# Optimization experiments

Measured on AMD Instinct MI355X. Metric: run time of the kernel, lower is better.

Reference implementation:

```python
import jax, jax.numpy as jnp
import numpy as np

N_NODES = 100000
N_EDGES = 1600000
IN_C = 128
DIM = 64
OUT_C = 64
BN_EPS = 1e-5


def _batchnorm(x, g, b):
    # training-mode BatchNorm1d: batch mean, biased variance
    m = jnp.mean(x, axis=0)
    v = jnp.var(x, axis=0)
    return (x - m) * jax.lax.rsqrt(v + BN_EPS) * g + b


def setup_inputs() -> dict:
    key = jax.random.key(0)
    ks = jax.random.split(key, 16)
    s = lambda fan: 1.0 / np.sqrt(fan)
    inp = {
        "X": jax.random.normal(ks[0], (N_NODES, IN_C), dtype=jnp.float32),
        "edge_index": jax.random.randint(ks[1], (2, N_EDGES), 0, N_NODES, dtype=jnp.int32),
        "edge_attr": jax.random.normal(ks[2], (N_EDGES, 1), dtype=jnp.float32),
        # bn_in over in_channels
        "bn_in_g": jnp.ones((IN_C,), jnp.float32),
        "bn_in_b": jnp.zeros((IN_C,), jnp.float32),
        # layer 0: edge lin 1->IN_C, node MLP IN_C->DIM
        "We0": jax.random.normal(ks[3], (1, IN_C), jnp.float32) * s(1),
        "be0": jnp.zeros((IN_C,), jnp.float32),
        "W0": jax.random.normal(ks[4], (IN_C, DIM), jnp.float32) * s(IN_C),
        "b0": jnp.zeros((DIM,), jnp.float32),
        "bn0_g": jnp.ones((DIM,), jnp.float32),
        "bn0_b": jnp.zeros((DIM,), jnp.float32),
        # layer 1: edge lin 1->DIM, node MLP DIM->DIM
        "We1": jax.random.normal(ks[5], (1, DIM), jnp.float32) * s(1),
        "be1": jnp.zeros((DIM,), jnp.float32),
        "W1": jax.random.normal(ks[6], (DIM, DIM), jnp.float32) * s(DIM),
        "b1": jnp.zeros((DIM,), jnp.float32),
        "bn1_g": jnp.ones((DIM,), jnp.float32),
        "bn1_b": jnp.zeros((DIM,), jnp.float32),
        # fc1: DIM->OUT_C, no bias
        "Wfc": jax.random.normal(ks[7], (DIM, OUT_C), jnp.float32) * s(DIM),
    }
    return inp


def reference(X, edge_index, edge_attr,
              bn_in_g, bn_in_b,
              We0, be0, W0, b0, bn0_g, bn0_b,
              We1, be1, W1, b1, bn1_g, bn1_b,
              Wfc):
    n = X.shape[0]
    src, dst = edge_index[0], edge_index[1]

    def gine(x, We, be, W, b):
        # GINEConv with eps=0: tanh(Linear(x + sum_j relu(x_j + lin(e_ij))))
        e = edge_attr @ We + be            # [E, C]
        msg = jax.nn.relu(x[src] + e)      # gather + edge-add + relu
        agg = jax.ops.segment_sum(msg, dst, num_segments=n)  # scatter-sum
        return jnp.tanh((x + agg) @ W + b)

    x = _batchnorm(X, bn_in_g, bn_in_b)
    h1 = _batchnorm(gine(x, We0, be0, W0, b0), bn0_g, bn0_b)
    h2 = _batchnorm(gine(h1, We1, be1, W1, b1), bn1_g, bn1_b)
    h3 = jnp.tanh(h2 @ Wfc)
    return jnp.concatenate([h1, h2, h3], axis=-1)  # [N, DIM+DIM+OUT_C]
```

## Files before the change

### kernel.cpp

```cpp
#include <hip/hip_runtime.h>
#include <hip/hip_fp16.h>
#include <math.h>
#include <stdint.h>

#define NN 100000
#define NE 1600000
#define INC 128
#define DIM 64
#define EPS 1e-5f
#define SB 512
#define NREP 8
#define NPART 8
#define PART_SZ ((NN + NPART - 1) / NPART)

struct __align__(8)  half4 { __half2 a, b; };
struct __align__(16) half8 { __half2 a, b, c, d; };

__global__ __launch_bounds__(256) void stats_hist_kernel(const float* __restrict__ X,
        const int* __restrict__ dst, int* __restrict__ counts,
        double* __restrict__ sum_out, double* __restrict__ sq_out) {
    __shared__ double ls[256], lq[256];
    if (blockIdx.x < SB) {
        int c  = threadIdx.x & 127;
        int rl = threadIdx.x >> 7;
        int row = blockIdx.x * 2 + rl;
        const int rstride = SB * 2;
        double s = 0.0, q = 0.0;
        for (int r = row; r < NN; r += rstride) {
            double v = (double)X[(size_t)r * INC + c];
            s += v; q += v * v;
        }
        ls[threadIdx.x] = s; lq[threadIdx.x] = q;
        __syncthreads();
        if (rl == 0) {
            s += ls[128 + c]; q += lq[128 + c];
            int rep = blockIdx.x & (NREP - 1);
            atomicAdd(&sum_out[rep * INC + c], s);
            atomicAdd(&sq_out[rep * INC + c], q);
        }
    } else {
        int e = (blockIdx.x - SB) * 256 + threadIdx.x;
        if (e < NE) atomicAdd(&counts[dst[e]], 1);
    }
}

template<int C>
__device__ inline void bn_fold_rep(int t, const double* dsum, const double* dsq,
                                   const float* g, const float* b, float* sc_s, float* sh_s) {
    if (t < C) {
        double s = 0.0, q = 0.0;
        #pragma unroll
        for (int r = 0; r < NREP; r++) { s += dsum[r * C + t]; q += dsq[r * C + t]; }
        double m = s / (double)NN;
        double v = q / (double)NN - m * m;
        double sc = (double)g[t] / sqrt(v + (double)EPS);
        sc_s[t] = (float)sc;
        sh_s[t] = (float)((double)b[t] - m * sc);
    }
}

__global__ __launch_bounds__(256) void xhat_half_kernel(const float* __restrict__ X,
        const double* __restrict__ dsum, const double* __restrict__ dsq,
        const float* __restrict__ g, const float* __restrict__ b,
        __half* __restrict__ Xh) {
    __shared__ float sc_s[INC], sh_s[INC];
    bn_fold_rep<INC>(threadIdx.x, dsum, dsq, g, b, sc_s, sh_s);
    __syncthreads();
    size_t i = (size_t)blockIdx.x * 256 + threadIdx.x;
    size_t e4 = i * 4;
    if (e4 >= (size_t)NN * INC) return;
    int c = (int)(e4 & 127);
    float4 x = *(const float4*)(X + e4);
    half4 h;
    h.a = __floats2half2_rn(fmaf(x.x, sc_s[c], sh_s[c]), fmaf(x.y, sc_s[c + 1], sh_s[c + 1]));
    h.b = __floats2half2_rn(fmaf(x.z, sc_s[c + 2], sh_s[c + 2]), fmaf(x.w, sc_s[c + 3], sh_s[c + 3]));
    *(half4*)(Xh + e4) = h;
}

__global__ __launch_bounds__(1024) void scan1_kernel(const int* __restrict__ counts,
                                                     int* __restrict__ offs, int* __restrict__ bsums) {
    __shared__ int tmp[2][1024];
    int t = threadIdx.x;
    int g = blockIdx.x * 1024 + t;
    int v = (g < NN) ? counts[g] : 0;
    tmp[0][t] = v;
    __syncthreads();
    int pin = 0;
    for (int d = 1; d < 1024; d <<= 1) {
        int x = tmp[pin][t] + ((t >= d) ? tmp[pin][t - d] : 0);
        tmp[pin ^ 1][t] = x;
        pin ^= 1;
        __syncthreads();
    }
    int incl = tmp[pin][t];
    if (g < NN) offs[g] = incl - v;
    if (t == 1023) bsums[blockIdx.x] = incl;
}

__global__ __launch_bounds__(128) void scan2_kernel(int* __restrict__ bsums, int nb) {
    __shared__ int tmp[2][128];
    int t = threadIdx.x;
    int v = (t < nb) ? bsums[t] : 0;
    tmp[0][t] = v;
    __syncthreads();
    int pin = 0;
    for (int d = 1; d < 128; d <<= 1) {
        int x = tmp[pin][t] + ((t >= d) ? tmp[pin][t - d] : 0);
        tmp[pin ^ 1][t] = x;
        pin ^= 1;
        __syncthreads();
    }
    if (t < nb) bsums[t] = tmp[pin][t] - v;
}

__global__ __launch_bounds__(256) void scan3_kernel(int* __restrict__ offs, const int* __restrict__ bsums,
                                                    int* __restrict__ cursor) {
    int g = blockIdx.x * 256 + threadIdx.x;
    if (g < NN) {
        int o = offs[g] + bsums[g >> 10];
        offs[g] = o;
        cursor[g] = o;
    }
    if (g == 0) offs[NN] = NE;
}

__global__ __launch_bounds__(256) void scatter_kernel(const int* __restrict__ src, const int* __restrict__ dst,
                                                      const float* __restrict__ ea, int* __restrict__ cursor,
                                                      int2* __restrict__ src_ea) {
    const int p = blockIdx.x & (NPART - 1);
    const int blk = blockIdx.x >> 3;
    const int nblk = gridDim.x >> 3;
    const int lo = p * PART_SZ;
    const int hi = min(NN, lo + PART_SZ);
    for (int e = blk * 256 + threadIdx.x; e < NE; e += nblk * 256) {
        int d = dst[e];
        if (d >= lo && d < hi) {
            int pos = atomicAdd(&cursor[d], 1);
            src_ea[pos] = make_int2(src[e], __float_as_int(ea[e]));
        }
    }
}

__global__ __launch_bounds__(512, 8) void gine0_kernel(const float* __restrict__ X,
        const __half* __restrict__ Xh,
        const int* __restrict__ offs, const int2* __restrict__ src_ea,
        const double* __restrict__ dsum, const double* __restrict__ dsq,
        const float* __restrict__ g, const float* __restrict__ b,
        const float* __restrict__ We, const float* __restrict__ be,
        const float* __restrict__ W, const float* __restrict__ bvec,
        __half* __restrict__ t1h, double* __restrict__ dsum0, double* __restrict__ dsq0) {
    __shared__ __align__(16) float  u_s[32][INC + 4];
    __shared__ __align__(16) __half w_sh[DIM][INC + 8];
    __shared__ float sc_s[INC], sh_s[INC];
    const int t = threadIdx.x;
    const int row0 = blockIdx.x * 32;
    bn_fold_rep<INC>(t, dsum, dsq, g, b, sc_s, sh_s);
    for (int i = t; i < INC * DIM; i += 512) {
        int k = i >> 6, c = i & 63;
        w_sh[c][k] = __float2half_rn(W[i]);
    }
    __syncthreads();
    const int wid = t >> 6, l = t & 63;
    const int quarter = l >> 4;
    const int c8 = (l & 15) * 8;
    float4 wv0 = *(const float4*)(We + c8);
    float4 wv1 = *(const float4*)(We + c8 + 4);
    float4 bv0 = *(const float4*)(be + c8);
    float4 bv1 = *(const float4*)(be + c8 + 4);

    #define G0_ACC(vh, av)  do { \
        float2 f0 = __half22float2((vh).a), f1 = __half22float2((vh).b); \
        float2 f2 = __half22float2((vh).c), f3 = __half22float2((vh).d); \
        a0 += fmaxf(f0.x + fmaf((av), wv0.x, bv0.x), 0.f); \
        a1 += fmaxf(f0.y + fmaf((av), wv0.y, bv0.y), 0.f); \
        a2 += fmaxf(f1.x + fmaf((av), wv0.z, bv0.z), 0.f); \
        a3 += fmaxf(f1.y + fmaf((av), wv0.w, bv0.w), 0.f); \
        a4 += fmaxf(f2.x + fmaf((av), wv1.x, bv1.x), 0.f); \
        a5 += fmaxf(f2.y + fmaf((av), wv1.y, bv1.y), 0.f); \
        a6 += fmaxf(f3.x + fmaf((av), wv1.z, bv1.z), 0.f); \
        a7 += fmaxf(f3.y + fmaf((av), wv1.w, bv1.w), 0.f); \
    } while (0)

    for (int nn = 0; nn < 4; ++nn) {
        int r = wid * 4 + nn;
        int n = row0 + r;
        float a0 = 0.f, a1 = 0.f, a2 = 0.f, a3 = 0.f, a4 = 0.f, a5 = 0.f, a6 = 0.f, a7 = 0.f;
        if (n < NN) {
            int beg = offs[n], end = offs[n + 1];
            for (int base = beg; base < end; base += 64) {
                int j = base + l;
                int2 p = (j < end) ? src_ea[j] : make_int2(0, 0);
                float avf = __int_as_float(p.y);
                int cnt = min(64, end - base);
                int tt = 0;
                for (; tt + 8 <= cnt; tt += 8) {
                    int e0 = tt + quarter, e1 = tt + 4 + quarter;
                    int s0 = __shfl(p.x, e0), s1 = __shfl(p.x, e1);
                    float av0 = __shfl(avf, e0), av1 = __shfl(avf, e1);
                    half8 v0 = *(const half8*)(Xh + (size_t)s0 * INC + c8);
                    half8 v1 = *(const half8*)(Xh + (size_t)s1 * INC + c8);
                    G0_ACC(v0, av0); G0_ACC(v1, av1);
                }
                for (; tt < cnt; tt += 4) {
                    int e0 = tt + quarter;
                    int es = min(e0, cnt - 1);
                    int s0 = __shfl(p.x, es);
                    float av0 = __shfl(avf, es);
                    if (e0 < cnt) {
                        half8 v0 = *(const half8*)(Xh + (size_t)s0 * INC + c8);
                        G0_ACC(v0, av0);
                    }
                }
            }
        }
        a0 += __shfl_xor(a0, 16); a0 += __shfl_xor(a0, 32);
        a1 += __shfl_xor(a1, 16); a1 += __shfl_xor(a1, 32);
        a2 += __shfl_xor(a2, 16); a2 += __shfl_xor(a2, 32);
        a3 += __shfl_xor(a3, 16); a3 += __shfl_xor(a3, 32);
        a4 += __shfl_xor(a4, 16); a4 += __shfl_xor(a4, 32);
        a5 += __shfl_xor(a5, 16); a5 += __shfl_xor(a5, 32);
        a6 += __shfl_xor(a6, 16); a6 += __shfl_xor(a6, 32);
        a7 += __shfl_xor(a7, 16); a7 += __shfl_xor(a7, 32);
        if (quarter == 0) {
            if (n < NN) {
                float4 x0 = *(const float4*)(X + (size_t)n * INC + c8);
                float4 x1 = *(const float4*)(X + (size_t)n * INC + c8 + 4);
                a0 += fmaf(x0.x, sc_s[c8],     sh_s[c8]);
                a1 += fmaf(x0.y, sc_s[c8 + 1], sh_s[c8 + 1]);
                a2 += fmaf(x0.z, sc_s[c8 + 2], sh_s[c8 + 2]);
                a3 += fmaf(x0.w, sc_s[c8 + 3], sh_s[c8 + 3]);
                a4 += fmaf(x1.x, sc_s[c8 + 4], sh_s[c8 + 4]);
                a5 += fmaf(x1.y, sc_s[c8 + 5], sh_s[c8 + 5]);
                a6 += fmaf(x1.z, sc_s[c8 + 6], sh_s[c8 + 6]);
                a7 += fmaf(x1.w, sc_s[c8 + 7], sh_s[c8 + 7]);
            }
            *(float4*)&u_s[r][c8]     = make_float4(a0, a1, a2, a3);
            *(float4*)&u_s[r][c8 + 4] = make_float4(a4, a5, a6, a7);
        }
    }
    #undef G0_ACC
    __syncthreads();
    const int cc = t & 15;
    const int rg = t >> 4;
    float acc0 = bvec[cc], acc1 = bvec[cc + 16], acc2 = bvec[cc + 32], acc3 = bvec[cc + 48];
    #pragma unroll 2
    for (int k = 0; k < INC; k += 8) {
        float4 ua = *(const float4*)&u_s[rg][k];
        float4 ub = *(const float4*)&u_s[rg][k + 4];
        half8 w0 = *(const half8*)&w_sh[cc][k];
        half8 w1 = *(const half8*)&w_sh[cc + 16][k];
        half8 w2 = *(const half8*)&w_sh[cc + 32][k];
        half8 w3 = *(const half8*)&w_sh[cc + 48][k];
        float2 p;
        p = __half22float2(w0.a); acc0 = fmaf(ua.x, p.x, fmaf(ua.y, p.y, acc0));
        p = __half22float2(w0.b); acc0 = fmaf(ua.z, p.x, fmaf(ua.w, p.y, acc0));
        p = __half22float2(w0.c); acc0 = fmaf(ub.x, p.x, fmaf(ub.y, p.y, acc0));
        p = __half22float2(w0.d); acc0 = fmaf(ub.z, p.x, fmaf(ub.w, p.y, acc0));
        p = __half22float2(w1.a); acc1 = fmaf(ua.x, p.x, fmaf(ua.y, p.y, acc1));
        p = __half22float2(w1.b); acc1 = fmaf(ua.z, p.x, fmaf(ua.w, p.y, acc1));
        p = __half22float2(w1.c); acc1 = fmaf(ub.x, p.x, fmaf(ub.y, p.y, acc1));
        p = __half22float2(w1.d); acc1 = fmaf(ub.z, p.x, fmaf(ub.w, p.y, acc1));
        p = __half22float2(w2.a); acc2 = fmaf(ua.x, p.x, fmaf(ua.y, p.y, acc2));
        p = __half22float2(w2.b); acc2 = fmaf(ua.z, p.x, fmaf(ua.w, p.y, acc2));
        p = __half22float2(w2.c); acc2 = fmaf(ub.x, p.x, fmaf(ub.y, p.y, acc2));
        p = __half22float2(w2.d); acc2 = fmaf(ub.z, p.x, fmaf(ub.w, p.y, acc2));
        p = __half22float2(w3.a); acc3 = fmaf(ua.x, p.x, fmaf(ua.y, p.y, acc3));
        p = __half22float2(w3.b); acc3 = fmaf(ua.z, p.x, fmaf(ua.w, p.y, acc3));
        p = __half22float2(w3.c); acc3 = fmaf(ub.x, p.x, fmaf(ub.y, p.y, acc3));
        p = __half22float2(w3.d); acc3 = fmaf(ub.z, p.x, fmaf(ub.w, p.y, acc3));
    }
    int rr = row0 + rg;
    float t0 = tanhf(acc0), t1v = tanhf(acc1), t2v = tanhf(acc2), t3v = tanhf(acc3);
    if (rr < NN) {
        __half* op = t1h + (size_t)rr * DIM;
        op[cc]      = __float2half_rn(t0);
        op[cc + 16] = __float2half_rn(t1v);
        op[cc + 32] = __float2half_rn(t2v);
        op[cc + 48] = __float2half_rn(t3v);
    }
    __syncthreads();
    float* red_s = (float*)u_s;
    float* red_q = red_s + 2048;
    bool ok = (rr < NN);
    red_s[rg * 64 + cc]      = ok ? t0 : 0.f;
    red_s[rg * 64 + cc + 16] = ok ? t1v : 0.f;
    red_s[rg * 64 + cc + 32] = ok ? t2v : 0.f;
    red_s[rg * 64 + cc + 48] = ok ? t3v : 0.f;
    red_q[rg * 64 + cc]      = ok ? t0 * t0 : 0.f;
    red_q[rg * 64 + cc + 16] = ok ? t1v * t1v : 0.f;
    red_q[rg * 64 + cc + 32] = ok ? t2v * t2v : 0.f;
    red_q[rg * 64 + cc + 48] = ok ? t3v * t3v : 0.f;
    __syncthreads();
    if (t < 64) {
        float s = 0.f, q = 0.f;
        #pragma unroll
        for (int i = 0; i < 32; i++) { s += red_s[i * 64 + t]; q += red_q[i * 64 + t]; }
        int rep = blockIdx.x & (NREP - 1);
        atomicAdd(&dsum0[rep * DIM + t], (double)s);
        atomicAdd(&dsq0[rep * DIM + t], (double)q);
    }
}

__global__ __launch_bounds__(512) void gine1_kernel(const __half* __restrict__ t1h,
        const int* __restrict__ offs, const int2* __restrict__ src_ea,
        const double* __restrict__ dsum, const double* __restrict__ dsq,
        const float* __restrict__ g, const float* __restrict__ b,
        const float* __restrict__ We, const float* __restrict__ be,
        const float* __restrict__ W, const float* __restrict__ bvec,
        float* __restrict__ out, double* __restrict__ dsum1, double* __restrict__ dsq1) {
    __shared__ __align__(16) float u_s[64][DIM + 4];
    __shared__ __align__(16) float w_s[DIM][DIM + 4];
    __shared__ float sc_s[DIM], sh_s[DIM];
    const int t = threadIdx.x;
    const int row0 = blockIdx.x * 64;
    bn_fold_rep<DIM>(t, dsum, dsq, g, b, sc_s, sh_s);
    for (int i = t; i < DIM * DIM; i += 512) {
        int k = i >> 6, c = i & 63;
        w_s[c][k] = W[i];
    }
    __syncthreads();
    const int wid = t >> 6, l = t & 63;
    const int quarter = l >> 4;
    const int c4 = (l & 15) * 4;
    float4 wv = *(const float4*)(We + c4);
    float4 bv = *(const float4*)(be + c4);
    float4 sc4 = *(const float4*)(sc_s + c4);
    float4 sh4 = *(const float4*)(sh_s + c4);

    #define G1_ACC(vh, av)  do { \
        float2 f00 = __half22float2((vh).a), f01 = __half22float2((vh).b); \
        a0 += fmaxf(fmaf(f00.x, sc4.x, sh4.x) + fmaf((av), wv.x, bv.x), 0.f); \
        a1 += fmaxf(fmaf(f00.y, sc4.y, sh4.y) + fmaf((av), wv.y, bv.y), 0.f); \
        a2 += fmaxf(fmaf(f01.x, sc4.z, sh4.z) + fmaf((av), wv.z, bv.z), 0.f); \
        a3 += fmaxf(fmaf(f01.y, sc4.w, sh4.w) + fmaf((av), wv.w, bv.w), 0.f); \
    } while (0)

    for (int nn = 0; nn < 8; ++nn) {
        int r = wid * 8 + nn;
        int n = row0 + r;
        float a0 = 0.f, a1 = 0.f, a2 = 0.f, a3 = 0.f;
        if (n < NN) {
            int beg = offs[n], end = offs[n + 1];
            for (int base = beg; base < end; base += 64) {
                int j = base + l;
                int2 p = (j < end) ? src_ea[j] : make_int2(0, 0);
                float avf = __int_as_float(p.y);
                int cnt = min(64, end - base);
                int tt = 0;
                for (; tt + 8 <= cnt; tt += 8) {
                    int e0 = tt + quarter, e1 = tt + 4 + quarter;
                    int s0 = __shfl(p.x, e0), s1 = __shfl(p.x, e1);
                    float av0 = __shfl(avf, e0), av1 = __shfl(avf, e1);
                    half4 v0 = *(const half4*)(t1h + (size_t)s0 * DIM + c4);
                    half4 v1 = *(const half4*)(t1h + (size_t)s1 * DIM + c4);
                    G1_ACC(v0, av0); G1_ACC(v1, av1);
                }
                for (; tt < cnt; tt += 4) {
                    int e0 = tt + quarter;
                    int es = min(e0, cnt - 1);
                    int s0 = __shfl(p.x, es);
                    float av0 = __shfl(avf, es);
                    if (e0 < cnt) {
                        half4 v0 = *(const half4*)(t1h + (size_t)s0 * DIM + c4);
                        G1_ACC(v0, av0);
                    }
                }
            }
        }
        a0 += __shfl_xor(a0, 16); a0 += __shfl_xor(a0, 32);
        a1 += __shfl_xor(a1, 16); a1 += __shfl_xor(a1, 32);
        a2 += __shfl_xor(a2, 16); a2 += __shfl_xor(a2, 32);
        a3 += __shfl_xor(a3, 16); a3 += __shfl_xor(a3, 32);
        if (quarter == 0) {
            if (n < NN) {
                half4 h = *(const half4*)(t1h + (size_t)n * DIM + c4);
                float2 f0 = __half22float2(h.a), f1 = __half22float2(h.b);
                float h0 = fmaf(f0.x, sc4.x, sh4.x);
                float h1 = fmaf(f0.y, sc4.y, sh4.y);
                float h2 = fmaf(f1.x, sc4.z, sh4.z);
                float h3 = fmaf(f1.y, sc4.w, sh4.w);
                *(float4*)(out + (size_t)n * 192 + c4) = make_float4(h0, h1, h2, h3);
                a0 += h0; a1 += h1; a2 += h2; a3 += h3;
            }
            *(float4*)&u_s[r][c4] = make_float4(a0, a1, a2, a3);
        }
    }
    #undef G1_ACC
    __syncthreads();
    const int cc = t & 15;
    const int r0 = (t >> 4) * 2;
    float acc[2][4];
    #pragma unroll
    for (int j = 0; j < 4; j++) {
        float bj = bvec[cc + 16 * j];
        acc[0][j] = bj; acc[1][j] = bj;
    }
    #pragma unroll 4
    for (int k = 0; k < DIM; k += 4) {
        float4 w0 = *(const float4*)&w_s[cc][k];
        float4 w1 = *(const float4*)&w_s[cc + 16][k];
        float4 w2 = *(const float4*)&w_s[cc + 32][k];
        float4 w3 = *(const float4*)&w_s[cc + 48][k];
        #pragma unroll
        for (int i = 0; i < 2; i++) {
            float4 u = *(const float4*)&u_s[r0 + i][k];
            acc[i][0] = fmaf(u.x, w0.x, fmaf(u.y, w0.y, fmaf(u.z, w0.z, fmaf(u.w, w0.w, acc[i][0]))));
            acc[i][1] = fmaf(u.x, w1.x, fmaf(u.y, w1.y, fmaf(u.z, w1.z, fmaf(u.w, w1.w, acc[i][1]))));
            acc[i][2] = fmaf(u.x, w2.x, fmaf(u.y, w2.y, fmaf(u.z, w2.z, fmaf(u.w, w2.w, acc[i][2]))));
            acc[i][3] = fmaf(u.x, w3.x, fmaf(u.y, w3.y, fmaf(u.z, w3.z, fmaf(u.w, w3.w, acc[i][3]))));
        }
    }
    float tv[2][4];
    #pragma unroll
    for (int i = 0; i < 2; i++) {
        int rr = row0 + r0 + i;
        #pragma unroll
        for (int j = 0; j < 4; j++) tv[i][j] = tanhf(acc[i][j]);
        if (rr < NN) {
            float* op = out + (size_t)rr * 192 + 64;
            #pragma unroll
            for (int j = 0; j < 4; j++) op[cc + 16 * j] = tv[i][j];
        }
    }
    __syncthreads();
    float* red_s = (float*)w_s;
    float* red_q = red_s + 2048;
    const int rgp = t >> 4;
    bool ok0 = (row0 + r0 < NN), ok1 = (row0 + r0 + 1 < NN);
    #pragma unroll
    for (int j = 0; j < 4; j++) {
        float v0 = ok0 ? tv[0][j] : 0.f;
        float v1 = ok1 ? tv[1][j] : 0.f;
        red_s[rgp * 64 + cc + 16 * j] = v0 + v1;
        red_q[rgp * 64 + cc + 16 * j] = v0 * v0 + v1 * v1;
    }
    __syncthreads();
    if (t < 64) {
        float s = 0.f, q = 0.f;
        #pragma unroll
        for (int i = 0; i < 32; i++) { s += red_s[i * 64 + t]; q += red_q[i * 64 + t]; }
        int rep = blockIdx.x & (NREP - 1);
        atomicAdd(&dsum1[rep * DIM + t], (double)s);
        atomicAdd(&dsq1[rep * DIM + t], (double)q);
    }
}

__global__ __launch_bounds__(256) void fc_kernel(float* __restrict__ io,
        const double* __restrict__ dsum, const double* __restrict__ dsq,
        const float* __restrict__ g, const float* __restrict__ b,
        const float* __restrict__ W) {
    __shared__ __align__(16) float u_s[64][DIM + 4];
    __shared__ __align__(16) float w_s[DIM][DIM + 4];
    __shared__ float sc_s[DIM], sh_s[DIM];
    const int t = threadIdx.x;
    const int row0 = blockIdx.x * 64;
    bn_fold_rep<DIM>(t, dsum, dsq, g, b, sc_s, sh_s);
    __syncthreads();
    for (int i = t; i < DIM * DIM; i += 256) {
        int k = i >> 6, c = i & 63;
        w_s[c][k] = W[i];
    }
    for (int i = t; i < 64 * DIM; i += 256) {
        int r = i >> 6, k = i & 63;
        int rr = row0 + r;
        float v = 0.f;
        if (rr < NN) {
            size_t idx = (size_t)rr * 192 + 64 + k;
            v = fmaf(io[idx], sc_s[k], sh_s[k]);
            io[idx] = v;
        }
        u_s[r][k] = v;
    }
    __syncthreads();
    const int cc = t & 15;
    const int r0 = (t >> 4) << 2;
    float acc[4][4];
    #pragma unroll
    for (int j = 0; j < 4; j++) { acc[0][j] = 0.f; acc[1][j] = 0.f; acc[2][j] = 0.f; acc[3][j] = 0.f; }
    #pragma unroll 4
    for (int k = 0; k < DIM; k += 4) {
        float4 w0 = *(const float4*)&w_s[cc][k];
        float4 w1 = *(const float4*)&w_s[cc + 16][k];
        float4 w2 = *(const float4*)&w_s[cc + 32][k];
        float4 w3 = *(const float4*)&w_s[cc + 48][k];
        #pragma unroll
        for (int i = 0; i < 4; i++) {
            float4 u = *(const float4*)&u_s[r0 + i][k];
            acc[i][0] = fmaf(u.x, w0.x, fmaf(u.y, w0.y, fmaf(u.z, w0.z, fmaf(u.w, w0.w, acc[i][0]))));
            acc[i][1] = fmaf(u.x, w1.x, fmaf(u.y, w1.y, fmaf(u.z, w1.z, fmaf(u.w, w1.w, acc[i][1]))));
            acc[i][2] = fmaf(u.x, w2.x, fmaf(u.y, w2.y, fmaf(u.z, w2.z, fmaf(u.w, w2.w, acc[i][2]))));
            acc[i][3] = fmaf(u.x, w3.x, fmaf(u.y, w3.y, fmaf(u.z, w3.z, fmaf(u.w, w3.w, acc[i][3]))));
        }
    }
    #pragma unroll
    for (int i = 0; i < 4; i++) {
        int rr = row0 + r0 + i;
        if (rr < NN) {
            #pragma unroll
            for (int j = 0; j < 4; j++)
                io[(size_t)rr * 192 + 128 + cc + 16 * j] = tanhf(acc[i][j]);
        }
    }
}

extern "C" void kernel_launch(void* const* d_in, const int* in_sizes, int n_in,
                              void* d_out, int out_size, void* d_ws, size_t ws_size,
                              hipStream_t stream) {
    const float* X      = (const float*)d_in[0];
    const int*   ei     = (const int*)  d_in[1];
    const float* ea     = (const float*)d_in[2];
    const float* bng    = (const float*)d_in[3];
    const float* bnb    = (const float*)d_in[4];
    const float* We0    = (const float*)d_in[5];
    const float* be0    = (const float*)d_in[6];
    const float* W0     = (const float*)d_in[7];
    const float* b0     = (const float*)d_in[8];
    const float* bn0g   = (const float*)d_in[9];
    const float* bn0b   = (const float*)d_in[10];
    const float* We1    = (const float*)d_in[11];
    const float* be1    = (const float*)d_in[12];
    const float* W1     = (const float*)d_in[13];
    const float* b1     = (const float*)d_in[14];
    const float* bn1g   = (const float*)d_in[15];
    const float* bn1b   = (const float*)d_in[16];
    const float* Wfc    = (const float*)d_in[17];

    const int* src = ei;
    const int* dst = ei + NE;
    float* out = (float*)d_out;

    int2*   src_ea  = (int2*)d_ws;
    __half* t1h     = (__half*)(src_ea + NE);
    __half* Xh      = t1h + (size_t)NN * DIM;
    int*    counts  = (int*)(Xh + (size_t)NN * INC);
    int*    offs    = counts + NN;
    int*    cursor  = offs + NN + 1;
    int*    bsums   = cursor + NN;
    double* dstats = (double*)(((uintptr_t)(bsums + 128) + 15) & ~(uintptr_t)15);
    double* dsum_in = dstats;
    double* dsq_in  = dsum_in + NREP * INC;
    double* dsum0   = dsq_in + NREP * INC;
    double* dsq0    = dsum0 + NREP * DIM;
    double* dsum1   = dsq0 + NREP * DIM;
    double* dsq1    = dsum1 + NREP * DIM;
    const size_t nstats = (size_t)NREP * (2 * INC + 4 * DIM);

    hipMemsetAsync(counts, 0, NN * sizeof(int), stream);
    hipMemsetAsync(dstats, 0, nstats * sizeof(double), stream);

    stats_hist_kernel<<<SB + (NE + 255) / 256, 256, 0, stream>>>(X, dst, counts, dsum_in, dsq_in);

    xhat_half_kernel<<<(NN * INC / 4 + 255) / 256, 256, 0, stream>>>(X, dsum_in, dsq_in, bng, bnb, Xh);

    const int NB = (NN + 1023) / 1024;
    scan1_kernel<<<NB, 1024, 0, stream>>>(counts, offs, bsums);
    scan2_kernel<<<1, 128, 0, stream>>>(bsums, NB);
    scan3_kernel<<<(NN + 255) / 256, 256, 0, stream>>>(offs, bsums, cursor);
    scatter_kernel<<<2048, 256, 0, stream>>>(src, dst, ea, cursor, src_ea);

    gine0_kernel<<<(NN + 31) / 32, 512, 0, stream>>>(X, Xh, offs, src_ea, dsum_in, dsq_in, bng, bnb,
                                                     We0, be0, W0, b0, t1h, dsum0, dsq0);

    gine1_kernel<<<(NN + 63) / 64, 512, 0, stream>>>(t1h, offs, src_ea, dsum0, dsq0, bn0g, bn0b,
                                                     We1, be1, W1, b1, out, dsum1, dsq1);

    fc_kernel<<<(NN + 63) / 64, 256, 0, stream>>>(out, dsum1, dsq1, bn1g, bn1b, Wfc);
}
```

Baseline: 442.8 us.

## Replicate degree histogram and accumulate layer-0 messages in packed fp16

The degree histogram is split into NREP replicated copies chosen by block index, so atomics from different blocks hit different copies. The first scan sums the copies back together. The layer-0 gather loop now computes the edge embedding, ReLU and accumulation in packed half2 arithmetic (v_pk_max_f16, hfma2) instead of converting to fp32. This cuts ALU work per edge, but accumulating sums of about 16 or more messages in fp16 loses precision and risks tolerance failures. The larger counts buffer also needs a larger memset and more reads in the scan.

```diff
diff --git a/kernel.cpp b/kernel.cpp
--- a/kernel.cpp
+++ b/kernel.cpp
@@ -15,6 +15,12 @@
 
 struct __align__(8)  half4 { __half2 a, b; };
 struct __align__(16) half8 { __half2 a, b, c, d; };
+
+__device__ inline __half2 h2max(__half2 a, __half2 b) {
+    __half2 r;
+    asm("v_pk_max_f16 %0, %1, %2" : "=v"(r) : "v"(a), "v"(b));
+    return r;
+}
 
 __global__ __launch_bounds__(256) void stats_hist_kernel(const float* __restrict__ X,
         const int* __restrict__ dst, int* __restrict__ counts,
@@ -39,8 +45,9 @@
             atomicAdd(&sq_out[rep * INC + c], q);
         }
     } else {
-        int e = (blockIdx.x - SB) * 256 + threadIdx.x;
-        if (e < NE) atomicAdd(&counts[dst[e]], 1);
+        int bb = blockIdx.x - SB;
+        int e = bb * 256 + threadIdx.x;
+        if (e < NE) atomicAdd(&counts[(bb & (NREP - 1)) * NN + dst[e]], 1);
     }
 }
 
@@ -82,7 +89,11 @@
     __shared__ int tmp[2][1024];
     int t = threadIdx.x;
     int g = blockIdx.x * 1024 + t;
-    int v = (g < NN) ? counts[g] : 0;
+    int v = 0;
+    if (g < NN) {
+        #pragma unroll
+        for (int r = 0; r < NREP; r++) v += counts[r * NN + g];
+    }
     tmp[0][t] = v;
     __syncthreads();
     int pin = 0;
@@ -163,28 +174,27 @@
     const int wid = t >> 6, l = t & 63;
     const int quarter = l >> 4;
     const int c8 = (l & 15) * 8;
-    float4 wv0 = *(const float4*)(We + c8);
-    float4 wv1 = *(const float4*)(We + c8 + 4);
-    float4 bv0 = *(const float4*)(be + c8);
-    float4 bv1 = *(const float4*)(be + c8 + 4);
-
-    #define G0_ACC(vh, av)  do { \
-        float2 f0 = __half22float2((vh).a), f1 = __half22float2((vh).b); \
-        float2 f2 = __half22float2((vh).c), f3 = __half22float2((vh).d); \
-        a0 += fmaxf(f0.x + fmaf((av), wv0.x, bv0.x), 0.f); \
-        a1 += fmaxf(f0.y + fmaf((av), wv0.y, bv0.y), 0.f); \
-        a2 += fmaxf(f1.x + fmaf((av), wv0.z, bv0.z), 0.f); \
-        a3 += fmaxf(f1.y + fmaf((av), wv0.w, bv0.w), 0.f); \
-        a4 += fmaxf(f2.x + fmaf((av), wv1.x, bv1.x), 0.f); \
-        a5 += fmaxf(f2.y + fmaf((av), wv1.y, bv1.y), 0.f); \
-        a6 += fmaxf(f3.x + fmaf((av), wv1.z, bv1.z), 0.f); \
-        a7 += fmaxf(f3.y + fmaf((av), wv1.w, bv1.w), 0.f); \
+    const __half2 z2 = __float2half2_rn(0.f);
+    __half2 wvh0 = __floats2half2_rn(We[c8],     We[c8 + 1]);
+    __half2 wvh1 = __floats2half2_rn(We[c8 + 2], We[c8 + 3]);
+    __half2 wvh2 = __floats2half2_rn(We[c8 + 4], We[c8 + 5]);
+    __half2 wvh3 = __floats2half2_rn(We[c8 + 6], We[c8 + 7]);
+    __half2 bvh0 = __floats2half2_rn(be[c8],     be[c8 + 1]);
+    __half2 bvh1 = __floats2half2_rn(be[c8 + 2], be[c8 + 3]);
+    __half2 bvh2 = __floats2half2_rn(be[c8 + 4], be[c8 + 5]);
+    __half2 bvh3 = __floats2half2_rn(be[c8 + 6], be[c8 + 7]);
+
+    #define G0_ACC(vh, av2)  do { \
+        ah0 = __hadd2(ah0, h2max(__hadd2((vh).a, __hfma2((av2), wvh0, bvh0)), z2)); \
+        ah1 = __hadd2(ah1, h2max(__hadd2((vh).b, __hfma2((av2), wvh1, bvh1)), z2)); \
+        ah2 = __hadd2(ah2, h2max(__hadd2((vh).c, __hfma2((av2), wvh2, bvh2)), z2)); \
+        ah3 = __hadd2(ah3, h2max(__hadd2((vh).d, __hfma2((av2), wvh3, bvh3)), z2)); \
     } while (0)
 
     for (int nn = 0; nn < 4; ++nn) {
         int r = wid * 4 + nn;
         int n = row0 + r;
-        float a0 = 0.f, a1 = 0.f, a2 = 0.f, a3 = 0.f, a4 = 0.f, a5 = 0.f, a6 = 0.f, a7 = 0.f;
+        __half2 ah0 = z2, ah1 = z2, ah2 = z2, ah3 = z2;
         if (n < NN) {
             int beg = offs[n], end = offs[n + 1];
             for (int base = beg; base < end; base += 64) {
@@ -199,7 +209,9 @@
                     float av0 = __shfl(avf, e0), av1 = __shfl(avf, e1);
                     half8 v0 = *(const half8*)(Xh + (size_t)s0 * INC + c8);
                     half8 v1 = *(const half8*)(Xh + (size_t)s1 * INC + c8);
-                    G0_ACC(v0, av0); G0_ACC(v1, av1);
+                    __half2 a2_0 = __half2half2(__float2half_rn(av0));
+                    __half2 a2_1 = __half2half2(__float2half_rn(av1));
+                    G0_ACC(v0, a2_0); G0_ACC(v1, a2_1);
                 }
                 for (; tt < cnt; tt += 4) {
                     int e0 = tt + quarter;
@@ -208,11 +220,16 @@
                     float av0 = __shfl(avf, es);
                     if (e0 < cnt) {
                         half8 v0 = *(const half8*)(Xh + (size_t)s0 * INC + c8);
-                        G0_ACC(v0, av0);
+                        __half2 a2_0 = __half2half2(__float2half_rn(av0));
+                        G0_ACC(v0, a2_0);
                     }
                 }
             }
         }
+        float2 p0 = __half22float2(ah0), p1 = __half22float2(ah1);
+        float2 p2 = __half22float2(ah2), p3 = __half22float2(ah3);
+        float a0 = p0.x, a1 = p0.y, a2 = p1.x, a3 = p1.y;
+        float a4 = p2.x, a5 = p2.y, a6 = p3.x, a7 = p3.y;
         a0 += __shfl_xor(a0, 16); a0 += __shfl_xor(a0, 32);
         a1 += __shfl_xor(a1, 16); a1 += __shfl_xor(a1, 32);
         a2 += __shfl_xor(a2, 16); a2 += __shfl_xor(a2, 32);
@@ -533,7 +550,7 @@
     __half* t1h     = (__half*)(src_ea + NE);
     __half* Xh      = t1h + (size_t)NN * DIM;
     int*    counts  = (int*)(Xh + (size_t)NN * INC);
-    int*    offs    = counts + NN;
+    int*    offs    = counts + (size_t)NREP * NN;
     int*    cursor  = offs + NN + 1;
     int*    bsums   = cursor + NN;
     double* dstats = (double*)(((uintptr_t)(bsums + 128) + 15) & ~(uintptr_t)15);
@@ -545,7 +562,7 @@
     double* dsq1    = dsum1 + NREP * DIM;
     const size_t nstats = (size_t)NREP * (2 * INC + 4 * DIM);
 
-    hipMemsetAsync(counts, 0, NN * sizeof(int), stream);
+    hipMemsetAsync(counts, 0, (size_t)NREP * NN * sizeof(int), stream);
     hipMemsetAsync(dstats, 0, nstats * sizeof(double), stream);
 
     stats_hist_kernel<<<SB + (NE + 255) / 256, 256, 0, stream>>>(X, dst, counts, dsum_in, dsq_in);
```

Result: faster. 428.3 us (-3.3%).
